# Optimization experiments

Hardware: AMD Instinct MI355X
Metric: run time of the kernel (lower is better)

The kernel has to match this reference:

```python
import jax, jax.numpy as jnp
import numpy as np

N_HARMONIC = 6
CONCAT = (3,)  # cfg.append_distance: concat embedding after this layer index
N_LAYERS = 8


def harmonic_embedding(x):
    # x: [N, 3] -> [N, 6*2*3 + 3] = [N, 39]
    freqs = 2.0 ** jnp.arange(N_HARMONIC, dtype=x.dtype)  # omega0 = 1.0, logspace
    embed = (x[..., None] * freqs).reshape(*x.shape[:-1], -1)  # [N, 18]
    return jnp.concatenate([jnp.sin(embed), jnp.cos(embed), x], axis=-1)


def setup_inputs() -> dict:
    key = jax.random.key(0)
    N, H, E = 262144, 256, 39
    ks = jax.random.split(key, 11)
    inp = {"points": jax.random.normal(ks[0], (N, 3), dtype=jnp.float32)}
    in_dims = [E, H, H, H, E + H, H, H, H]  # skip-concat before layer 4
    for i, d_in in enumerate(in_dims):
        scale = 1.0 / np.sqrt(d_in)
        inp[f"w{i}"] = jax.random.normal(ks[i + 1], (d_in, H), dtype=jnp.float32) * scale
        inp[f"b{i}"] = jnp.zeros((H,), dtype=jnp.float32)
    inp["wsdf"] = jax.random.normal(ks[9], (H, 1), dtype=jnp.float32) * (1.0 / np.sqrt(H))
    inp["bsdf"] = jnp.zeros((1,), dtype=jnp.float32)
    return inp


def reference(points, w0, b0, w1, b1, w2, b2, w3, b3, w4, b4, w5, b5, w6, b6, w7, b7, wsdf, bsdf):
    ws = [w0, w1, w2, w3, w4, w5, w6, w7]
    bs = [b0, b1, b2, b3, b4, b5, b6, b7]
    emb = harmonic_embedding(points.reshape(-1, 3))  # [N, 39]
    x = emb
    for i in range(N_LAYERS):
        x = jax.nn.relu(x @ ws[i] + bs[i])
        if i in CONCAT:
            x = jnp.concatenate([emb, x], axis=-1)  # torch.cat([add, xyz])
    return x @ wsdf + bsdf  # [N, 1] signed distance
```

## Files before the change

### kernel.cpp

```cpp
#include <hip/hip_runtime.h>
#include <hip/hip_fp16.h>

typedef _Float16 f16x8 __attribute__((ext_vector_type(8)));
typedef _Float16 f16x4 __attribute__((ext_vector_type(4)));
typedef _Float16 f16x2 __attribute__((ext_vector_type(2)));
typedef float    f32x16 __attribute__((ext_vector_type(16)));
typedef float    f32x4 __attribute__((ext_vector_type(4)));

#define SH 264
#define SE 56

struct LayerPtrs {
  const float* w[8];
  const float* b[8];
};

__global__ void prep_weights(LayerPtrs P, f16x8* __restrict__ wf) {
  int gid = blockIdx.x * 256 + threadIdx.x;
  if (gid >= 60416) return;
  const int OFF[9] = {0,1536,9728,17920,26112,35840,44032,52224,60416};
  int l = 0;
  while (gid >= OFF[l+1]) ++l;
  int f = gid - OFF[l];
  int lane = f & 63;
  int t = f >> 6;
  int mtile = t & 7;
  int kc = t >> 3;
  int col = mtile * 32 + (lane & 31);
  int kb  = (lane >> 5) * 8;
  const float* w = P.w[l];
  f16x8 v;
#pragma unroll
  for (int j = 0; j < 8; ++j) {
    float x = 0.f;
    if (l == 4) {
      if (kc < 3) {
        int k = kc * 16 + kb + j;
        if (k < 39) x = w[k * 256 + col];
      } else {
        int k = (kc - 3) * 16 + kb + j;
        x = w[(39 + k) * 256 + col];
      }
    } else if (l == 0) {
      int k = kc * 16 + kb + j;
      if (k < 39) x = w[k * 256 + col];
    } else {
      int k = kc * 16 + kb + j;
      x = w[k * 256 + col];
    }
    v[j] = (_Float16)x;
  }
  wf[gid] = v;
}

#define MFMA __builtin_amdgcn_mfma_f32_32x32x16_f16

__device__ __forceinline__ void mfma8(f16x8 a0, f16x8 a1, f16x8 a2, f16x8 a3,
                                      f16x8 v0, f16x8 v1, f32x16 acc[4][2]) {
  acc[0][0] = MFMA(a0, v0, acc[0][0], 0, 0, 0);
  acc[0][1] = MFMA(a0, v1, acc[0][1], 0, 0, 0);
  acc[1][0] = MFMA(a1, v0, acc[1][0], 0, 0, 0);
  acc[1][1] = MFMA(a1, v1, acc[1][1], 0, 0, 0);
  acc[2][0] = MFMA(a2, v0, acc[2][0], 0, 0, 0);
  acc[2][1] = MFMA(a2, v1, acc[2][1], 0, 0, 0);
  acc[3][0] = MFMA(a3, v0, acc[3][0], 0, 0, 0);
  acc[3][1] = MFMA(a3, v1, acc[3][1], 0, 0, 0);
}

__device__ __forceinline__ void mfma8_z(f16x8 a0, f16x8 a1, f16x8 a2, f16x8 a3,
                                        f16x8 v0, f16x8 v1, f32x16 acc[4][2]) {
  const f32x16 z = {};
  acc[0][0] = MFMA(a0, v0, z, 0, 0, 0);
  acc[0][1] = MFMA(a0, v1, z, 0, 0, 0);
  acc[1][0] = MFMA(a1, v0, z, 0, 0, 0);
  acc[1][1] = MFMA(a1, v1, z, 0, 0, 0);
  acc[2][0] = MFMA(a2, v0, z, 0, 0, 0);
  acc[2][1] = MFMA(a2, v1, z, 0, 0, 0);
  acc[3][0] = MFMA(a3, v0, z, 0, 0, 0);
  acc[3][1] = MFMA(a3, v1, z, 0, 0, 0);
}

template<int NKC, bool FIRST, int RSTRIDE>
__device__ __forceinline__ void mm(const f16x8* __restrict__ wb,
                                   const char* __restrict__ r0,
                                   int hoff, f32x16 acc[4][2]) {
  f16x8 a0 = wb[0], a1 = wb[64], a2 = wb[128], a3 = wb[192];
  const char* rp = r0 + hoff;
  f16x8 v0 = *(const f16x8*)(rp);
  f16x8 v1 = *(const f16x8*)(rp + RSTRIDE);
  {
    const f16x8* wn = wb + 512;
    f16x8 na0 = wn[0], na1 = wn[64], na2 = wn[128], na3 = wn[192];
    f16x8 nv0 = *(const f16x8*)(rp + 32);
    f16x8 nv1 = *(const f16x8*)(rp + RSTRIDE + 32);
    if (FIRST) mfma8_z(a0, a1, a2, a3, v0, v1, acc);
    else       mfma8(a0, a1, a2, a3, v0, v1, acc);
    a0 = na0; a1 = na1; a2 = na2; a3 = na3; v0 = nv0; v1 = nv1;
  }
  const f16x8* wp = wb + 1024;
  rp += 64;
#pragma unroll 2
  for (int kc = 1; kc < NKC - 1; ++kc) {
    f16x8 na0 = wp[0], na1 = wp[64], na2 = wp[128], na3 = wp[192];
    f16x8 nv0 = *(const f16x8*)(rp);
    f16x8 nv1 = *(const f16x8*)(rp + RSTRIDE);
    mfma8(a0, a1, a2, a3, v0, v1, acc);
    a0 = na0; a1 = na1; a2 = na2; a3 = na3; v0 = nv0; v1 = nv1;
    wp += 512; rp += 32;
  }
  mfma8(a0, a1, a2, a3, v0, v1, acc);
}

__device__ __forceinline__ f16x4 relu_cvt4(float a0, float a1, float a2, float a3) {
  f16x2 lo = __builtin_bit_cast(f16x2, __builtin_amdgcn_cvt_pkrtz(a0, a1));
  f16x2 hi = __builtin_bit_cast(f16x2, __builtin_amdgcn_cvt_pkrtz(a2, a3));
  union { f16x4 v; f16x2 h[2]; } u;
  u.h[0] = lo; u.h[1] = hi;
  f16x4 z = {};
  return __builtin_elementwise_max(u.v, z);
}

__device__ __forceinline__ void store_epi(f32x16 acc[4][2],
                                          const float* __restrict__ bias,
                                          int wg_h, int wg_p, int p0, int h,
                                          _Float16* __restrict__ Hs) {
  char* base = (char*)Hs + (wg_p * 64 + p0) * (SH * 2);
#pragma unroll
  for (int mt = 0; mt < 4; ++mt) {
#pragma unroll
    for (int g = 0; g < 4; ++g) {
      f32x4 q = *(const f32x4*)&bias[wg_h * 128 + mt * 32 + 8 * g + 4 * h];
      int bc = 256 * wg_h + 64 * mt + 16 * g + 8 * h;
#pragma unroll
      for (int nt = 0; nt < 2; ++nt) {
        f16x4 o = relu_cvt4(acc[mt][nt][4 * g + 0] + q[0],
                            acc[mt][nt][4 * g + 1] + q[1],
                            acc[mt][nt][4 * g + 2] + q[2],
                            acc[mt][nt][4 * g + 3] + q[3]);
        *(f16x4*)(base + nt * 32 * (SH * 2) + bc) = o;
      }
    }
  }
}

__device__ __forceinline__ void emb_channel(_Float16* __restrict__ Erow,
                                            int c, float x) {
  _Float16 sv[6], cv[6];
  float fr = 1.f;
#pragma unroll
  for (int k = 0; k < 6; ++k) {
    float e = x * fr;
    sv[k] = (_Float16)__sinf(e);
    cv[k] = (_Float16)__cosf(e);
    fr *= 2.f;
  }
#pragma unroll
  for (int k = 0; k < 6; k += 2) {
    f16x2 s2 = {sv[k], sv[k + 1]};
    f16x2 c2 = {cv[k], cv[k + 1]};
    *(f16x2*)&Erow[6 * c + k]      = s2;
    *(f16x2*)&Erow[18 + 6 * c + k] = c2;
  }
  Erow[36 + c] = (_Float16)x;
}

__global__ __launch_bounds__(256, 2)
void mlp_fused(const float* __restrict__ points,
               LayerPtrs P,
               const f16x8* __restrict__ wf,
               const float* __restrict__ wsdf,
               const float* __restrict__ bsdf,
               float* __restrict__ out) {
  __shared__ __align__(16) _Float16 Hs[128 * SH];
  __shared__ __align__(16) _Float16 Es[128 * SE];
  const int tid = threadIdx.x;
  const int blk = blockIdx.x;

  const int lane = tid & 63;
  const int w    = tid >> 6;
  const int wg_h = w >> 1;
  const int wg_p = w & 1;
  const int p0   = lane & 31;
  const int h    = lane >> 5;
  const int hoff = 16 * h;

  const f16x8* wb = wf + wg_h * 256 + lane;

  {
    int p = tid & 127, part = tid >> 7;
    _Float16* Erow = &Es[p * SE];
    const float* pp = &points[(blk * 128 + p) * 3];
    if (part == 0) {
      emb_channel(Erow, 0, pp[0]);
      emb_channel(Erow, 1, pp[1]);
    } else {
      emb_channel(Erow, 2, pp[2]);
      Erow[39] = (_Float16)0.f;
      f16x4 z4 = {};
      *(f16x4*)&Erow[40] = z4;
      *(f16x4*)&Erow[44] = z4;
      *(f16x4*)&Erow[48] = z4;
      *(f16x4*)&Erow[52] = z4;
    }
  }
  __syncthreads();

  const char* hR = (const char*)Hs + (wg_p * 64 + p0) * (SH * 2);
  const char* eR = (const char*)Es + (wg_p * 64 + p0) * (SE * 2);

  f32x16 acc[4][2];

  mm<3, true, 32 * SE * 2>(wb, eR, hoff, acc);
  store_epi(acc, P.b[0], wg_h, wg_p, p0, h, Hs);
  __syncthreads();

  const int WOFF[8] = {0, 1536, 9728, 17920, 26112, 35840, 44032, 52224};

#pragma unroll
  for (int l = 1; l < 4; ++l) {
    mm<16, true, 32 * SH * 2>(wb + WOFF[l], hR, hoff, acc);
    __syncthreads();
    store_epi(acc, P.b[l], wg_h, wg_p, p0, h, Hs);
    __syncthreads();
  }

  {
    mm<3, true, 32 * SE * 2>(wb + 26112, eR, hoff, acc);
    mm<16, false, 32 * SH * 2>(wb + 27648, hR, hoff, acc);
    __syncthreads();
    store_epi(acc, P.b[4], wg_h, wg_p, p0, h, Hs);
    __syncthreads();
  }

#pragma unroll
  for (int l = 5; l < 7; ++l) {
    mm<16, true, 32 * SH * 2>(wb + WOFF[l], hR, hoff, acc);
    __syncthreads();
    store_epi(acc, P.b[l], wg_h, wg_p, p0, h, Hs);
    __syncthreads();
  }

  mm<16, true, 32 * SH * 2>(wb + 52224, hR, hoff, acc);
  {
    float part0 = 0.f, part1 = 0.f;
    const float* b7 = P.b[7];
#pragma unroll
    for (int mt = 0; mt < 4; ++mt) {
#pragma unroll
      for (int g = 0; g < 4; ++g) {
        int idx = wg_h * 128 + mt * 32 + 8 * g + 4 * h;
        f32x4 qb = *(const f32x4*)&b7[idx];
        f32x4 qw = *(const f32x4*)&wsdf[idx];
#pragma unroll
        for (int r = 0; r < 4; ++r) {
          part0 += fmaxf(acc[mt][0][4 * g + r] + qb[r], 0.f) * qw[r];
          part1 += fmaxf(acc[mt][1][4 * g + r] + qb[r], 0.f) * qw[r];
        }
      }
    }
    float* PB = (float*)Es;
    PB[(wg_h * 2 + h) * 128 + wg_p * 64 + p0]      = part0;
    PB[(wg_h * 2 + h) * 128 + wg_p * 64 + 32 + p0] = part1;
    __syncthreads();
    if (tid < 128) {
      float s = bsdf[0];
#pragma unroll
      for (int j = 0; j < 4; ++j) s += PB[j * 128 + tid];
      out[blk * 128 + tid] = s;
    }
  }
}

extern "C" void kernel_launch(void* const* d_in, const int* in_sizes, int n_in,
                              void* d_out, int out_size, void* d_ws, size_t ws_size,
                              hipStream_t stream) {
  const float* points = (const float*)d_in[0];
  LayerPtrs P;
  for (int i = 0; i < 8; ++i) {
    P.w[i] = (const float*)d_in[1 + 2 * i];
    P.b[i] = (const float*)d_in[2 + 2 * i];
  }
  const float* wsdf = (const float*)d_in[17];
  const float* bsdf = (const float*)d_in[18];
  f16x8* wf = (f16x8*)d_ws;

  int N = in_sizes[0] / 3;
  prep_weights<<<236, 256, 0, stream>>>(P, wf);
  mlp_fused<<<N / 128, 256, 0, stream>>>(points, P, wf, wsdf, bsdf, (float*)d_out);
}
```

Baseline: 322.4 us.

## Retile waves to 64 hidden units by 128 points to halve weight fetches

The four waves change from a 2x2 split (128 hidden units by 64 points each) to a 4x1 split (64 hidden units by all 128 points each). Each wave now loads two weight fragments per K-chunk instead of four, halving per-wave global/L2 weight traffic. In exchange, each wave reads four activation fragments from shared memory instead of two, doubling LDS reads. The weight prefetch is deepened to two K-chunks ahead, and the epilogue and final SDF reduction are rewritten for the new accumulator shape, with the reduction now summing eight partials per point.

```diff
diff --git a/kernel.cpp b/kernel.cpp
--- a/kernel.cpp
+++ b/kernel.cpp
@@ -55,60 +55,78 @@
 
 #define MFMA __builtin_amdgcn_mfma_f32_32x32x16_f16
 
-__device__ __forceinline__ void mfma8(f16x8 a0, f16x8 a1, f16x8 a2, f16x8 a3,
-                                      f16x8 v0, f16x8 v1, f32x16 acc[4][2]) {
+__device__ __forceinline__ void mfma8(f16x8 a0, f16x8 a1,
+                                      f16x8 v0, f16x8 v1, f16x8 v2, f16x8 v3,
+                                      f32x16 acc[2][4]) {
   acc[0][0] = MFMA(a0, v0, acc[0][0], 0, 0, 0);
   acc[0][1] = MFMA(a0, v1, acc[0][1], 0, 0, 0);
+  acc[0][2] = MFMA(a0, v2, acc[0][2], 0, 0, 0);
+  acc[0][3] = MFMA(a0, v3, acc[0][3], 0, 0, 0);
   acc[1][0] = MFMA(a1, v0, acc[1][0], 0, 0, 0);
   acc[1][1] = MFMA(a1, v1, acc[1][1], 0, 0, 0);
-  acc[2][0] = MFMA(a2, v0, acc[2][0], 0, 0, 0);
-  acc[2][1] = MFMA(a2, v1, acc[2][1], 0, 0, 0);
-  acc[3][0] = MFMA(a3, v0, acc[3][0], 0, 0, 0);
-  acc[3][1] = MFMA(a3, v1, acc[3][1], 0, 0, 0);
-}
-
-__device__ __forceinline__ void mfma8_z(f16x8 a0, f16x8 a1, f16x8 a2, f16x8 a3,
-                                        f16x8 v0, f16x8 v1, f32x16 acc[4][2]) {
+  acc[1][2] = MFMA(a1, v2, acc[1][2], 0, 0, 0);
+  acc[1][3] = MFMA(a1, v3, acc[1][3], 0, 0, 0);
+}
+
+__device__ __forceinline__ void mfma8_z(f16x8 a0, f16x8 a1,
+                                        f16x8 v0, f16x8 v1, f16x8 v2, f16x8 v3,
+                                        f32x16 acc[2][4]) {
   const f32x16 z = {};
   acc[0][0] = MFMA(a0, v0, z, 0, 0, 0);
   acc[0][1] = MFMA(a0, v1, z, 0, 0, 0);
+  acc[0][2] = MFMA(a0, v2, z, 0, 0, 0);
+  acc[0][3] = MFMA(a0, v3, z, 0, 0, 0);
   acc[1][0] = MFMA(a1, v0, z, 0, 0, 0);
   acc[1][1] = MFMA(a1, v1, z, 0, 0, 0);
-  acc[2][0] = MFMA(a2, v0, z, 0, 0, 0);
-  acc[2][1] = MFMA(a2, v1, z, 0, 0, 0);
-  acc[3][0] = MFMA(a3, v0, z, 0, 0, 0);
-  acc[3][1] = MFMA(a3, v1, z, 0, 0, 0);
+  acc[1][2] = MFMA(a1, v2, z, 0, 0, 0);
+  acc[1][3] = MFMA(a1, v3, z, 0, 0, 0);
 }
 
 template<int NKC, bool FIRST, int RSTRIDE>
 __device__ __forceinline__ void mm(const f16x8* __restrict__ wb,
                                    const char* __restrict__ r0,
-                                   int hoff, f32x16 acc[4][2]) {
-  f16x8 a0 = wb[0], a1 = wb[64], a2 = wb[128], a3 = wb[192];
-  const char* rp = r0 + hoff;
-  f16x8 v0 = *(const f16x8*)(rp);
-  f16x8 v1 = *(const f16x8*)(rp + RSTRIDE);
-  {
-    const f16x8* wn = wb + 512;
-    f16x8 na0 = wn[0], na1 = wn[64], na2 = wn[128], na3 = wn[192];
-    f16x8 nv0 = *(const f16x8*)(rp + 32);
-    f16x8 nv1 = *(const f16x8*)(rp + RSTRIDE + 32);
-    if (FIRST) mfma8_z(a0, a1, a2, a3, v0, v1, acc);
-    else       mfma8(a0, a1, a2, a3, v0, v1, acc);
-    a0 = na0; a1 = na1; a2 = na2; a3 = na3; v0 = nv0; v1 = nv1;
-  }
-  const f16x8* wp = wb + 1024;
-  rp += 64;
+                                   f32x16 acc[2][4]) {
+  f16x8 a00 = wb[0],   a01 = wb[64];
+  f16x8 a10 = wb[512], a11 = wb[576];
+  f16x8 v00 = *(const f16x8*)(r0);
+  f16x8 v01 = *(const f16x8*)(r0 + RSTRIDE);
+  f16x8 v02 = *(const f16x8*)(r0 + 2 * RSTRIDE);
+  f16x8 v03 = *(const f16x8*)(r0 + 3 * RSTRIDE);
+  {
+    f16x8 na0 = wb[1024], na1 = wb[1088];
+    f16x8 nv0 = *(const f16x8*)(r0 + 32);
+    f16x8 nv1 = *(const f16x8*)(r0 + RSTRIDE + 32);
+    f16x8 nv2 = *(const f16x8*)(r0 + 2 * RSTRIDE + 32);
+    f16x8 nv3 = *(const f16x8*)(r0 + 3 * RSTRIDE + 32);
+    if (FIRST) mfma8_z(a00, a01, v00, v01, v02, v03, acc);
+    else       mfma8 (a00, a01, v00, v01, v02, v03, acc);
+    a00 = a10; a01 = a11; a10 = na0; a11 = na1;
+    v00 = nv0; v01 = nv1; v02 = nv2; v03 = nv3;
+  }
+  const f16x8* wp = wb + 1536;
+  const char* rp  = r0 + 64;
 #pragma unroll 2
-  for (int kc = 1; kc < NKC - 1; ++kc) {
-    f16x8 na0 = wp[0], na1 = wp[64], na2 = wp[128], na3 = wp[192];
+  for (int kc = 1; kc <= NKC - 3; ++kc) {
+    f16x8 na0 = wp[0], na1 = wp[64];
     f16x8 nv0 = *(const f16x8*)(rp);
     f16x8 nv1 = *(const f16x8*)(rp + RSTRIDE);
-    mfma8(a0, a1, a2, a3, v0, v1, acc);
-    a0 = na0; a1 = na1; a2 = na2; a3 = na3; v0 = nv0; v1 = nv1;
+    f16x8 nv2 = *(const f16x8*)(rp + 2 * RSTRIDE);
+    f16x8 nv3 = *(const f16x8*)(rp + 3 * RSTRIDE);
+    mfma8(a00, a01, v00, v01, v02, v03, acc);
+    a00 = a10; a01 = a11; a10 = na0; a11 = na1;
+    v00 = nv0; v01 = nv1; v02 = nv2; v03 = nv3;
     wp += 512; rp += 32;
   }
-  mfma8(a0, a1, a2, a3, v0, v1, acc);
+  {
+    f16x8 nv0 = *(const f16x8*)(rp);
+    f16x8 nv1 = *(const f16x8*)(rp + RSTRIDE);
+    f16x8 nv2 = *(const f16x8*)(rp + 2 * RSTRIDE);
+    f16x8 nv3 = *(const f16x8*)(rp + 3 * RSTRIDE);
+    mfma8(a00, a01, v00, v01, v02, v03, acc);
+    a00 = a10; a01 = a11;
+    v00 = nv0; v01 = nv1; v02 = nv2; v03 = nv3;
+  }
+  mfma8(a00, a01, v00, v01, v02, v03, acc);
 }
 
 __device__ __forceinline__ f16x4 relu_cvt4(float a0, float a1, float a2, float a3) {
@@ -120,24 +138,23 @@
   return __builtin_elementwise_max(u.v, z);
 }
 
-__device__ __forceinline__ void store_epi(f32x16 acc[4][2],
+__device__ __forceinline__ void store_epi(f32x16 acc[2][4],
                                           const float* __restrict__ bias,
-                                          int wg_h, int wg_p, int p0, int h,
+                                          int wg, int p0, int h,
                                           _Float16* __restrict__ Hs) {
-  char* base = (char*)Hs + (wg_p * 64 + p0) * (SH * 2);
-#pragma unroll
-  for (int mt = 0; mt < 4; ++mt) {
+#pragma unroll
+  for (int mt = 0; mt < 2; ++mt) {
+    int hb = wg * 64 + mt * 32 + 4 * h;
 #pragma unroll
     for (int g = 0; g < 4; ++g) {
-      f32x4 q = *(const f32x4*)&bias[wg_h * 128 + mt * 32 + 8 * g + 4 * h];
-      int bc = 256 * wg_h + 64 * mt + 16 * g + 8 * h;
-#pragma unroll
-      for (int nt = 0; nt < 2; ++nt) {
+      f32x4 q = *(const f32x4*)&bias[hb + 8 * g];
+#pragma unroll
+      for (int nt = 0; nt < 4; ++nt) {
         f16x4 o = relu_cvt4(acc[mt][nt][4 * g + 0] + q[0],
                             acc[mt][nt][4 * g + 1] + q[1],
                             acc[mt][nt][4 * g + 2] + q[2],
                             acc[mt][nt][4 * g + 3] + q[3]);
-        *(f16x4*)(base + nt * 32 * (SH * 2) + bc) = o;
+        *(f16x4*)&Hs[(nt * 32 + p0) * SH + hb + 8 * g] = o;
       }
     }
   }
@@ -177,14 +194,11 @@
   const int blk = blockIdx.x;
 
   const int lane = tid & 63;
-  const int w    = tid >> 6;
-  const int wg_h = w >> 1;
-  const int wg_p = w & 1;
+  const int wg   = tid >> 6;
   const int p0   = lane & 31;
   const int h    = lane >> 5;
-  const int hoff = 16 * h;
-
-  const f16x8* wb = wf + wg_h * 256 + lane;
+
+  const f16x8* wb = wf + wg * 128 + lane;
 
   {
     int p = tid & 127, part = tid >> 7;
@@ -205,67 +219,68 @@
   }
   __syncthreads();
 
-  const char* hR = (const char*)Hs + (wg_p * 64 + p0) * (SH * 2);
-  const char* eR = (const char*)Es + (wg_p * 64 + p0) * (SE * 2);
-
-  f32x16 acc[4][2];
-
-  mm<3, true, 32 * SE * 2>(wb, eR, hoff, acc);
-  store_epi(acc, P.b[0], wg_h, wg_p, p0, h, Hs);
+  const char* hR = (const char*)Hs + (p0 * SH + 8 * h) * 2;
+  const char* eR = (const char*)Es + (p0 * SE + 8 * h) * 2;
+
+  f32x16 acc[2][4];
+
+  mm<3, true, 32 * SE * 2>(wb, eR, acc);
+  store_epi(acc, P.b[0], wg, p0, h, Hs);
   __syncthreads();
 
   const int WOFF[8] = {0, 1536, 9728, 17920, 26112, 35840, 44032, 52224};
 
 #pragma unroll
   for (int l = 1; l < 4; ++l) {
-    mm<16, true, 32 * SH * 2>(wb + WOFF[l], hR, hoff, acc);
-    __syncthreads();
-    store_epi(acc, P.b[l], wg_h, wg_p, p0, h, Hs);
-    __syncthreads();
-  }
-
-  {
-    mm<3, true, 32 * SE * 2>(wb + 26112, eR, hoff, acc);
-    mm<16, false, 32 * SH * 2>(wb + 27648, hR, hoff, acc);
-    __syncthreads();
-    store_epi(acc, P.b[4], wg_h, wg_p, p0, h, Hs);
+    mm<16, true, 32 * SH * 2>(wb + WOFF[l], hR, acc);
+    __syncthreads();
+    store_epi(acc, P.b[l], wg, p0, h, Hs);
+    __syncthreads();
+  }
+
+  {
+    mm<3, true, 32 * SE * 2>(wb + 26112, eR, acc);
+    mm<16, false, 32 * SH * 2>(wb + 27648, hR, acc);
+    __syncthreads();
+    store_epi(acc, P.b[4], wg, p0, h, Hs);
     __syncthreads();
   }
 
 #pragma unroll
   for (int l = 5; l < 7; ++l) {
-    mm<16, true, 32 * SH * 2>(wb + WOFF[l], hR, hoff, acc);
-    __syncthreads();
-    store_epi(acc, P.b[l], wg_h, wg_p, p0, h, Hs);
-    __syncthreads();
-  }
-
-  mm<16, true, 32 * SH * 2>(wb + 52224, hR, hoff, acc);
-  {
-    float part0 = 0.f, part1 = 0.f;
+    mm<16, true, 32 * SH * 2>(wb + WOFF[l], hR, acc);
+    __syncthreads();
+    store_epi(acc, P.b[l], wg, p0, h, Hs);
+    __syncthreads();
+  }
+
+  mm<16, true, 32 * SH * 2>(wb + 52224, hR, acc);
+  {
+    float part[4] = {0.f, 0.f, 0.f, 0.f};
     const float* b7 = P.b[7];
 #pragma unroll
-    for (int mt = 0; mt < 4; ++mt) {
+    for (int mt = 0; mt < 2; ++mt) {
 #pragma unroll
       for (int g = 0; g < 4; ++g) {
-        int idx = wg_h * 128 + mt * 32 + 8 * g + 4 * h;
+        int idx = wg * 64 + mt * 32 + 8 * g + 4 * h;
         f32x4 qb = *(const f32x4*)&b7[idx];
         f32x4 qw = *(const f32x4*)&wsdf[idx];
 #pragma unroll
-        for (int r = 0; r < 4; ++r) {
-          part0 += fmaxf(acc[mt][0][4 * g + r] + qb[r], 0.f) * qw[r];
-          part1 += fmaxf(acc[mt][1][4 * g + r] + qb[r], 0.f) * qw[r];
-        }
+        for (int nt = 0; nt < 4; ++nt)
+#pragma unroll
+          for (int r = 0; r < 4; ++r)
+            part[nt] += fmaxf(acc[mt][nt][4 * g + r] + qb[r], 0.f) * qw[r];
       }
     }
     float* PB = (float*)Es;
-    PB[(wg_h * 2 + h) * 128 + wg_p * 64 + p0]      = part0;
-    PB[(wg_h * 2 + h) * 128 + wg_p * 64 + 32 + p0] = part1;
+#pragma unroll
+    for (int nt = 0; nt < 4; ++nt)
+      PB[(wg * 2 + h) * 128 + nt * 32 + p0] = part[nt];
     __syncthreads();
     if (tid < 128) {
       float s = bsdf[0];
 #pragma unroll
-      for (int j = 0; j < 4; ++j) s += PB[j * 128 + tid];
+      for (int j = 0; j < 8; ++j) s += PB[j * 128 + tid];
       out[blk * 128 + tid] = s;
     }
   }
```

Result: faster. 299.6 us (-7.1%).
